# Optimization experiments

Hardware: AMD Instinct MI355X
Metric: run time of the kernel (lower is better)

## Reference

```python
import jax, jax.numpy as jnp
import numpy as np

B, C, CI, H, W = 8, 1024, 512, 56, 56
BN_EPS = 1e-5


def _conv1x1(x, w, b):
    # x: [B,C,H,W], w: [O,C], b: [O] -> [B,O,H,W]
    return jnp.einsum('bchw,oc->bohw', x, w) + b[None, :, None, None]


def setup_inputs() -> dict:
    key = jax.random.key(0)
    ks = jax.random.split(key, 12)
    s = lambda k, shape: (jax.random.normal(k, shape, jnp.float32) * 0.02)
    return {
        'x': jax.random.normal(ks[0], (B, C, H, W), jnp.float32),
        'theta_w': s(ks[1], (CI, C)), 'theta_b': s(ks[2], (CI,)),
        'phi_w': s(ks[3], (CI, C)), 'phi_b': s(ks[4], (CI,)),
        'g_w': s(ks[5], (CI, C)), 'g_b': s(ks[6], (CI,)),
        'wz_w': s(ks[7], (C, CI)), 'wz_b': s(ks[8], (C,)),
        'bn_gamma': 1.0 + 0.1 * jax.random.normal(ks[9], (C,), jnp.float32),
        'bn_beta': s(ks[10], (C,)),
    }


def reference(x, theta_w, theta_b, phi_w, phi_b, g_w, g_b, wz_w, wz_b, bn_gamma, bn_beta):
    b, c, h, w = x.shape
    n = h * w
    # 1x1-conv projections, flattened to token sequences
    g_x = _conv1x1(x, g_w, g_b).reshape(b, -1, n).transpose(0, 2, 1)       # [B,N,CI]
    theta_x = _conv1x1(x, theta_w, theta_b).reshape(b, -1, n).transpose(0, 2, 1)  # [B,N,CI]
    phi_x = _conv1x1(x, phi_w, phi_b).reshape(b, -1, n)                     # [B,CI,N]
    # embedded-gaussian: f = theta @ phi^T, softmax over last dim
    f = jnp.einsum('bnc,bcm->bnm', theta_x, phi_x)                          # [B,N,N]
    attn = jax.nn.softmax(f, axis=-1)
    y = jnp.einsum('bnm,bmc->bnc', attn, g_x)                               # [B,N,CI]
    y = y.transpose(0, 2, 1).reshape(b, -1, h, w)                           # [B,CI,H,W]
    z = _conv1x1(y, wz_w, wz_b)                                             # [B,C,H,W]
    # BatchNorm2d in training mode: batch statistics over (B,H,W), biased var
    mean = z.mean(axis=(0, 2, 3))
    var = z.var(axis=(0, 2, 3))
    zn = (z - mean[None, :, None, None]) * jax.lax.rsqrt(var + BN_EPS)[None, :, None, None]
    zn = zn * bn_gamma[None, :, None, None] + bn_beta[None, :, None, None]
    return zn + x
```

## Files before the change

kernel.cpp:

```cpp
#include <hip/hip_runtime.h>
#include <cstdint>
#include <cstdio>

#define DEVINL __device__ __forceinline__

typedef _Float16 f16x8 __attribute__((ext_vector_type(8)));
typedef float    f32x4 __attribute__((ext_vector_type(4)));

static constexpr int B_  = 8;
static constexpr int C_  = 1024;
static constexpr int CI_ = 512;
static constexpr int N_  = 56 * 56;
static constexpr int NP  = 3328;
static constexpr float BN_EPS = 1e-5f;

DEVINL uint16_t f2h(float f) {
  union { _Float16 h; uint16_t u; } cv;
  cv.h = (_Float16)f;
  return cv.u;
}

DEVINL void async16(const void* g, void* lds) {
  __builtin_amdgcn_global_load_lds(
      (const __attribute__((address_space(1))) uint32_t*)g,
      (__attribute__((address_space(3))) uint32_t*)lds, 16, 0, 0);
}

template <int BIAS>
__global__ __launch_bounds__(512, 2) void gemm256(
    const uint16_t* __restrict__ A, const uint16_t* __restrict__ Bt,
    uint16_t* __restrict__ Cc, const float* __restrict__ bias,
    int K, int lda, int ldb, int ldc,
    long aBatch, long bBatch, long cBatch, int nbx, int nby, int colMajor) {
  __shared__ uint16_t lds[65536];

  const int nwg = gridDim.x, orig = blockIdx.x;
  const int q = nwg >> 3, r = nwg & 7, xcd = orig & 7, idx = orig >> 3;
  const int wgid = (xcd < r ? xcd * (q + 1) : r * (q + 1) + (xcd - r) * q) + idx;
  const int rest = wgid % (nbx * nby);
  const int bx = colMajor ? rest / nby : rest % nbx;
  const int by = colMajor ? rest % nby : rest / nbx;
  const int zb = wgid / (nbx * nby);

  const int tid = threadIdx.x, w = tid >> 6, l = tid & 63;
  const int wm = w >> 2, wn = w & 3, lr = l & 15, lg = l >> 4;

  const uint16_t* Ab = A + (long)zb * aBatch + (long)bx * 256 * lda;
  const uint16_t* Bb = Bt + (long)zb * bBatch + (long)by * 256 * ldb;

  const int NT = K >> 6;

  const int c0 = tid, c1 = 512 + tid;
  const long aoff0 = (long)(c0 >> 2) * lda + (((c0 & 3) ^ ((c0 >> 3) & 3)) * 8);
  const long aoff1 = (long)(c1 >> 2) * lda + (((c1 & 3) ^ ((c1 >> 3) & 3)) * 8);
  const long boff0 = (long)(c0 >> 2) * ldb + (((c0 & 3) ^ ((c0 >> 3) & 3)) * 8);
  const long boff1 = (long)(c1 >> 2) * ldb + (((c1 & 3) ^ ((c1 >> 3) & 3)) * 8);
  const int ldsW0 = (w * 64) * 8;
  const int ldsW1 = (512 + w * 64) * 8;

  auto stageA = [&](int t, int ks, int buf) {
    int tw = t; while (tw >= NT) tw -= NT;
    const uint16_t* src = Ab + tw * 64 + ks * 32;
    const int reg = (buf * 2 + ks) * 8192;
    async16(src + aoff0, &lds[reg + ldsW0]);
    async16(src + aoff1, &lds[reg + ldsW1]);
  };
  auto stageB = [&](int t, int ks, int buf) {
    int tw = t; while (tw >= NT) tw -= NT;
    const uint16_t* src = Bb + tw * 64 + ks * 32;
    const int reg = 32768 + (buf * 2 + ks) * 8192;
    async16(src + boff0, &lds[reg + ldsW0]);
    async16(src + boff1, &lds[reg + ldsW1]);
  };

  const int laneSwz = (lg ^ ((lr >> 1) & 3)) * 8;
  f32x4 acc[8][4] = {};
  f16x8 af[4], bf[4];

#define LOAD_A(b, ks, mh)                                                     \
  _Pragma("unroll") for (int i = 0; i < 4; ++i) {                             \
    const int row_ = wm * 128 + ((mh) * 4 + i) * 16 + lr;                     \
    af[i] = *reinterpret_cast<const f16x8*>(                                  \
        &lds[((b) * 2 + (ks)) * 8192 + row_ * 32 + laneSwz]);                 \
  }
#define LOAD_B(b, ks)                                                         \
  _Pragma("unroll") for (int i = 0; i < 4; ++i) {                             \
    const int row_ = wn * 64 + i * 16 + lr;                                   \
    bf[i] = *reinterpret_cast<const f16x8*>(                                  \
        &lds[32768 + ((b) * 2 + (ks)) * 8192 + row_ * 32 + laneSwz]);         \
  }
#define MFMA16(mh)                                                            \
  _Pragma("unroll") for (int i = 0; i < 4; ++i)                               \
  _Pragma("unroll") for (int j = 0; j < 4; ++j)                               \
    acc[(mh) * 4 + i][j] = __builtin_amdgcn_mfma_f32_16x16x32_f16(            \
        af[i], bf[j], acc[(mh) * 4 + i][j], 0, 0, 0);
#define WAIT_LGKM()                                       \
  asm volatile("s_waitcnt lgkmcnt(0)" ::: "memory");      \
  __builtin_amdgcn_sched_barrier(0);
#define WAIT_VM8()                                        \
  asm volatile("s_waitcnt vmcnt(8)" ::: "memory");        \
  __builtin_amdgcn_sched_barrier(0);

#define TILE(t, b)                                                            \
  {                                                                           \
                                                   \
    LOAD_B(b, 0); LOAD_A(b, 0, 0);                                            \
    stageA((t) + 1, 1, (b) ^ 1);                                              \
    __builtin_amdgcn_s_barrier(); WAIT_LGKM();                                \
    __builtin_amdgcn_s_setprio(1); MFMA16(0); __builtin_amdgcn_s_setprio(0);  \
    __builtin_amdgcn_s_barrier();                                             \
                                                   \
    LOAD_A(b, 0, 1);                                                          \
    stageB((t) + 1, 1, (b) ^ 1);                                              \
    __builtin_amdgcn_s_barrier(); WAIT_LGKM();                                \
    __builtin_amdgcn_s_setprio(1); MFMA16(1); __builtin_amdgcn_s_setprio(0);  \
    WAIT_VM8();                                                               \
    __builtin_amdgcn_s_barrier();                                             \
                                                   \
    LOAD_B(b, 1); LOAD_A(b, 1, 0);                                            \
    stageA((t) + 2, 0, (b));                                                  \
    __builtin_amdgcn_s_barrier(); WAIT_LGKM();                                \
    __builtin_amdgcn_s_setprio(1); MFMA16(0); __builtin_amdgcn_s_setprio(0);  \
    __builtin_amdgcn_s_barrier();                                             \
                                                   \
    LOAD_A(b, 1, 1);                                                          \
    stageB((t) + 2, 0, (b));                                                  \
    __builtin_amdgcn_s_barrier(); WAIT_LGKM();                                \
    __builtin_amdgcn_s_setprio(1); MFMA16(1); __builtin_amdgcn_s_setprio(0);  \
    WAIT_VM8();                                                               \
    __builtin_amdgcn_s_barrier();                                             \
  }

  stageA(0, 0, 0); stageB(0, 0, 0);
  stageA(0, 1, 0); stageB(0, 1, 0);
  stageA(1, 0, 1); stageB(1, 0, 1);
  WAIT_VM8();
  __builtin_amdgcn_s_barrier();

  const int NTE = NT & ~1;
  for (int tp = 0; tp < NTE; tp += 2) {
    TILE(tp, 0);
    TILE(tp + 1, 1);
  }
  if (NT & 1) TILE(NT - 1, 0);

#undef TILE
#undef LOAD_A
#undef LOAD_B
#undef MFMA16
#undef WAIT_LGKM
#undef WAIT_VM8

  uint16_t* Cp = Cc + (long)zb * cBatch + ((long)bx * 256) * ldc + (long)by * 256;
#pragma unroll
  for (int mf = 0; mf < 8; ++mf) {
#pragma unroll
    for (int nf = 0; nf < 4; ++nf) {
      const int col = wn * 64 + nf * 16 + lr;
      const f32x4 v = acc[mf][nf];
#pragma unroll
      for (int qq = 0; qq < 4; ++qq) {
        const int row = wm * 128 + mf * 16 + lg * 4 + qq;
        float val = v[qq];
        if constexpr (BIAS == 1) val += bias[bx * 256 + row];
        if constexpr (BIAS == 2) val += bias[by * 256 + col];
        Cp[(long)row * ldc + col] = f2h(val);
      }
    }
  }
}

__global__ __launch_bounds__(256) void transpose_cast(
    const float* __restrict__ x, uint16_t* __restrict__ xT) {
  __shared__ float t[32][33];
  const int b = blockIdx.z;
  const float* xb = x + (long)b * C_ * N_;
  uint16_t* xTb = xT + (long)b * NP * C_;
  const int n0 = blockIdx.x * 32, c0 = blockIdx.y * 32;
  const int tx = threadIdx.x & 31, ty = threadIdx.x >> 5;
#pragma unroll
  for (int i = 0; i < 4; ++i) {
    const int cc = c0 + ty + i * 8, nn = n0 + tx;
    t[ty + i * 8][tx] = (nn < N_) ? xb[(long)cc * N_ + nn] : 0.f;
  }
  __syncthreads();
#pragma unroll
  for (int i = 0; i < 4; ++i) {
    const int nn = n0 + ty + i * 8, cc = c0 + tx;
    xTb[(long)nn * C_ + cc] = f2h(t[tx][ty + i * 8]);
  }
}

__global__ __launch_bounds__(256) void cvt_f16_all(
    const float* __restrict__ s0, uint16_t* __restrict__ d0, int n0,
    const float* __restrict__ s1, uint16_t* __restrict__ d1, int n1,
    const float* __restrict__ s2, uint16_t* __restrict__ d2, int n2,
    const float* __restrict__ s3, uint16_t* __restrict__ d3, int n3) {
  const int stride = gridDim.x * 256;
  const int total = n0 + n1 + n2 + n3;
  for (int i = blockIdx.x * 256 + threadIdx.x; i < total; i += stride) {
    int j = i;
    if (j < n0) { d0[j] = f2h(s0[j]); continue; }
    j -= n0;
    if (j < n1) { d1[j] = f2h(s1[j]); continue; }
    j -= n1;
    if (j < n2) { d2[j] = f2h(s2[j]); continue; }
    j -= n2;
    d3[j] = f2h(s3[j]);
  }
}

__global__ __launch_bounds__(256) void concat_bias(
    const float* __restrict__ a, const float* __restrict__ b,
    float* __restrict__ d) {
  const int i = blockIdx.x * 256 + threadIdx.x;
  if (i < 512) d[i] = a[i];
  else if (i < 1024) d[i] = b[i - 512];
}

__global__ __launch_bounds__(256) void softmax_inplace(uint16_t* __restrict__ f) {
  const int row = blockIdx.x, tid = threadIdx.x;
  uint16_t* p = f + ((long)blockIdx.y * NP + row) * NP;
  __shared__ float buf[N_];
  __shared__ float red[8];
  float mx = -3.4e38f;
  for (int ch = tid; ch < N_ / 8; ch += 256) {
    const f16x8 v = *reinterpret_cast<const f16x8*>(p + ch * 8);
#pragma unroll
    for (int j = 0; j < 8; ++j) {
      const float fv = (float)v[j];
      buf[ch * 8 + j] = fv;
      mx = fmaxf(mx, fv);
    }
  }
  for (int o = 32; o; o >>= 1) mx = fmaxf(mx, __shfl_xor(mx, o));
  if ((tid & 63) == 0) red[tid >> 6] = mx;
  __syncthreads();
  mx = fmaxf(fmaxf(red[0], red[1]), fmaxf(red[2], red[3]));

  float s = 0.f;
  for (int i = tid; i < N_; i += 256) {
    const float e = __expf(buf[i] - mx);
    buf[i] = e;
    s += e;
  }
  for (int o = 32; o; o >>= 1) s += __shfl_xor(s, o);
  __syncthreads();
  if ((tid & 63) == 0) red[tid >> 6] = s;
  __syncthreads();
  const float rinv = 1.0f / (red[0] + red[1] + red[2] + red[3]);

  for (int ch = tid; ch < N_ / 8; ch += 256) {
    f16x8 o8;
#pragma unroll
    for (int j = 0; j < 8; ++j) o8[j] = (_Float16)(buf[ch * 8 + j] * rinv);
    *reinterpret_cast<f16x8*>(p + ch * 8) = o8;
  }
}

__global__ __launch_bounds__(256) void bn_stats(
    const _Float16* __restrict__ z, const float* __restrict__ gamma,
    const float* __restrict__ beta, float* __restrict__ ss) {
  const int c = blockIdx.x, tid = threadIdx.x;
  float sum = 0.f, sq = 0.f;
  for (int b = 0; b < B_; ++b) {
    const _Float16* zp = z + ((long)b * C_ + c) * NP;
    for (int ch = tid; ch < N_ / 8; ch += 256) {
      const f16x8 v = *(const f16x8*)(zp + ch * 8);
#pragma unroll
      for (int j = 0; j < 8; ++j) {
        const float fv = (float)v[j];
        sum += fv;
        sq += fv * fv;
      }
    }
  }
  for (int o = 32; o; o >>= 1) {
    sum += __shfl_xor(sum, o);
    sq += __shfl_xor(sq, o);
  }
  __shared__ float r1[8], r2[8];
  if ((tid & 63) == 0) { r1[tid >> 6] = sum; r2[tid >> 6] = sq; }
  __syncthreads();
  if (tid == 0) {
    sum = r1[0] + r1[1] + r1[2] + r1[3];
    sq  = r2[0] + r2[1] + r2[2] + r2[3];
    const float inv_n = 1.0f / (float)(B_ * N_);
    const float mean = sum * inv_n;
    const float var = sq * inv_n - mean * mean;
    const float sc = gamma[c] * rsqrtf(var + BN_EPS);
    ss[c] = sc;
    ss[C_ + c] = beta[c] - mean * sc;
  }
}

__global__ __launch_bounds__(256) void bn_apply(
    const _Float16* __restrict__ z, const float* __restrict__ x,
    const float* __restrict__ ss, float* __restrict__ out) {
  constexpr int CH = N_ / 8;
  const long nv = (long)B_ * C_ * CH;
  const long stride = (long)gridDim.x * 256;
  for (long v = (long)blockIdx.x * 256 + threadIdx.x; v < nv; v += stride) {
    const long row = v / CH;
    const int ch = (int)(v % CH);
    const int c = (int)(row % C_);
    const f16x8 zz = *(const f16x8*)(z + row * NP + ch * 8);
    const f32x4 x0 = *(const f32x4*)(x + row * (long)N_ + ch * 8);
    const f32x4 x1 = *(const f32x4*)(x + row * (long)N_ + ch * 8 + 4);
    const float sc = ss[c], sh = ss[C_ + c];
    f32x4 o0, o1;
#pragma unroll
    for (int j = 0; j < 4; ++j) o0[j] = (float)zz[j] * sc + sh + x0[j];
#pragma unroll
    for (int j = 0; j < 4; ++j) o1[j] = (float)zz[4 + j] * sc + sh + x1[j];
    __builtin_nontemporal_store(o0, (f32x4*)(out + row * (long)N_ + ch * 8));
    __builtin_nontemporal_store(o1, (f32x4*)(out + row * (long)N_ + ch * 8 + 4));
  }
}

extern "C" void kernel_launch(void* const* d_in, const int* in_sizes, int n_in,
                              void* d_out, int out_size, void* d_ws,
                              size_t ws_size, hipStream_t stream) {
  const float* x       = (const float*)d_in[0];
  const float* theta_w = (const float*)d_in[1];
  const float* theta_b = (const float*)d_in[2];
  const float* phi_w   = (const float*)d_in[3];
  const float* phi_b   = (const float*)d_in[4];
  const float* g_w     = (const float*)d_in[5];
  const float* g_b     = (const float*)d_in[6];
  const float* wz_w    = (const float*)d_in[7];
  const float* wz_b    = (const float*)d_in[8];
  const float* gamma   = (const float*)d_in[9];
  const float* beta    = (const float*)d_in[10];
  float* out = (float*)d_out;

  char* ws = (char*)d_ws;
  size_t off = 0;
  auto alloc = [&](size_t bytes) {
    void* p = ws + off;
    off += (bytes + 255) & ~(size_t)255;
    return p;
  };
  uint16_t* wfused = (uint16_t*)alloc((size_t)1024 * 1024 * 2);
  uint16_t* wg     = (uint16_t*)alloc((size_t)CI_ * C_ * 2);
  uint16_t* wzh    = (uint16_t*)alloc((size_t)C_ * CI_ * 2);
  float*    bfused = (float*)alloc((size_t)1024 * 4);
  uint16_t* projT  = (uint16_t*)alloc((size_t)B_ * NP * 1024 * 2);
  uint16_t* gbuf   = (uint16_t*)alloc((size_t)B_ * CI_ * NP * 2);
  uint16_t* ybuf   = (uint16_t*)alloc((size_t)B_ * NP * CI_ * 2);
  uint16_t* zbuf   = (uint16_t*)alloc((size_t)B_ * C_ * NP * 2);
  float*    ss     = (float*)alloc((size_t)C_ * 2 * 4);

  const size_t xTb = (size_t)B_ * NP * C_ * 2;
  const size_t fB  = (size_t)B_ * NP * NP * 2;
  uint16_t* xT    = (uint16_t*)alloc(fB > xTb ? fB : xTb);
  uint16_t* fattn = xT;
  if (off > ws_size) {
    fprintf(stderr, "kernel_launch: workspace too small: need %zu have %zu\n",
            off, ws_size);
    return;
  }

  cvt_f16_all<<<512, 256, 0, stream>>>(
      theta_w, wfused, CI_ * C_,
      phi_w, wfused + 512 * 1024, CI_ * C_,
      g_w, wg, CI_ * C_,
      wz_w, wzh, C_ * CI_);
  concat_bias<<<4, 256, 0, stream>>>(theta_b, phi_b, bfused);

  transpose_cast<<<dim3(NP / 32, C_ / 32, B_), 256, 0, stream>>>(x, xT);

  gemm256<2><<<dim3(B_ * NP / 256 * 4), 512, 0, stream>>>(
      xT, wfused, projT, bfused, C_, C_, C_, 1024,
      0, 0, 0, B_ * NP / 256, 4, 1);
  gemm256<1><<<dim3(2 * 13 * B_), 512, 0, stream>>>(
      wg, xT, gbuf, g_b, C_, C_, C_, NP,
      0, (long)NP * C_, (long)CI_ * NP, 2, 13, 0);

  gemm256<0><<<dim3(13 * 13 * B_), 512, 0, stream>>>(
      projT, projT + 512, fattn, nullptr, CI_, 1024, 1024, NP,
      (long)NP * 1024, (long)NP * 1024, (long)NP * NP, 13, 13, 0);
  softmax_inplace<<<dim3(N_, B_), 256, 0, stream>>>(fattn);

  gemm256<0><<<dim3(13 * 2 * B_), 512, 0, stream>>>(
      fattn, gbuf, ybuf, nullptr, N_, NP, NP, CI_,
      (long)NP * NP, (long)CI_ * NP, (long)NP * CI_, 13, 2, 1);

  gemm256<1><<<dim3(4 * 13 * B_), 512, 0, stream>>>(
      wzh, ybuf, zbuf, wz_b, CI_, CI_, CI_, NP,
      0, (long)NP * CI_, (long)C_ * NP, 4, 13, 0);

  bn_stats<<<C_, 256, 0, stream>>>((const _Float16*)zbuf, gamma, beta, ss);
  bn_apply<<<4096, 256, 0, stream>>>((const _Float16*)zbuf, x, ss, out);
}
```

Before: 508.1 us.

## Fuse softmax exponentiation into attention-value GEMM A-tile staging

The softmax pass no longer writes normalized probabilities back to the score matrix. It only computes the row max and the reciprocal sum. The attn@g GEMM now exponentiates the raw score tiles in LDS after they are staged, and scales its output rows by the reciprocal sum in the epilogue. This avoids one full read-modify-write of the B×N×N fp16 score matrix. The cost is an extra LDS pass with exp work and an added barrier per K sub-tile inside the GEMM main loop, and the padded score columns must now be safe to exponentiate.

```diff
diff --git a/kernel.cpp b/kernel.cpp
--- a/kernel.cpp
+++ b/kernel.cpp
@@ -26,12 +26,14 @@
       (__attribute__((address_space(3))) uint32_t*)lds, 16, 0, 0);
 }
 
-template <int BIAS>
+template <int BIAS, int EXPA>
 __global__ __launch_bounds__(512, 2) void gemm256(
     const uint16_t* __restrict__ A, const uint16_t* __restrict__ Bt,
     uint16_t* __restrict__ Cc, const float* __restrict__ bias,
     int K, int lda, int ldb, int ldc,
-    long aBatch, long bBatch, long cBatch, int nbx, int nby, int colMajor) {
+    long aBatch, long bBatch, long cBatch, int nbx, int nby, int colMajor,
+    const float* __restrict__ rowM, const float* __restrict__ rowScale,
+    long rmBatch) {
   __shared__ uint16_t lds[65536];
 
   const int nwg = gridDim.x, orig = blockIdx.x;
@@ -49,6 +51,15 @@
   const uint16_t* Bb = Bt + (long)zb * bBatch + (long)by * 256 * ldb;
 
   const int NT = K >> 6;
+
+  float mA0 = 0.f, mA1 = 0.f;
+  const float* rscB = nullptr;
+  if constexpr (EXPA) {
+    const float* rm = rowM + (long)zb * rmBatch + (long)bx * 256;
+    mA0 = rm[tid >> 2];
+    mA1 = rm[128 + (tid >> 2)];
+    rscB = rowScale + (long)zb * rmBatch + (long)bx * 256;
+  }
 
   const int c0 = tid, c1 = 512 + tid;
   const long aoff0 = (long)(c0 >> 2) * lda + (((c0 & 3) ^ ((c0 >> 3) & 3)) * 8);
@@ -100,9 +111,26 @@
 #define WAIT_VM8()                                        \
   asm volatile("s_waitcnt vmcnt(8)" ::: "memory");        \
   __builtin_amdgcn_sched_barrier(0);
+#define PREP(b, ks)                                                           \
+  if constexpr (EXPA) {                                                       \
+    const int base_ = ((b) * 2 + (ks)) * 8192;                                \
+    f16x8 v0_ = *reinterpret_cast<const f16x8*>(&lds[base_ + tid * 8]);       \
+    f16x8 v1_ = *reinterpret_cast<const f16x8*>(&lds[base_ + (512 + tid) * 8]);\
+    f16x8 o0_, o1_;                                                           \
+    _Pragma("unroll") for (int j = 0; j < 8; ++j) {                           \
+      o0_[j] = (_Float16)__expf((float)v0_[j] - mA0);                         \
+      o1_[j] = (_Float16)__expf((float)v1_[j] - mA1);                         \
+    }                                                                         \
+    *reinterpret_cast<f16x8*>(&lds[base_ + tid * 8]) = o0_;                   \
+    *reinterpret_cast<f16x8*>(&lds[base_ + (512 + tid) * 8]) = o1_;           \
+    asm volatile("s_waitcnt lgkmcnt(0)" ::: "memory");                        \
+    __builtin_amdgcn_sched_barrier(0);                                        \
+    __builtin_amdgcn_s_barrier();                                             \
+  }
 
 #define TILE(t, b)                                                            \
   {                                                                           \
+    PREP(b, 0)                                                                \
                                                    \
     LOAD_B(b, 0); LOAD_A(b, 0, 0);                                            \
     stageA((t) + 1, 1, (b) ^ 1);                                              \
@@ -116,6 +144,7 @@
     __builtin_amdgcn_s_setprio(1); MFMA16(1); __builtin_amdgcn_s_setprio(0);  \
     WAIT_VM8();                                                               \
     __builtin_amdgcn_s_barrier();                                             \
+    PREP(b, 1)                                                                \
                                                    \
     LOAD_B(b, 1); LOAD_A(b, 1, 0);                                            \
     stageA((t) + 2, 0, (b));                                                  \
@@ -145,6 +174,7 @@
   if (NT & 1) TILE(NT - 1, 0);
 
 #undef TILE
+#undef PREP
 #undef LOAD_A
 #undef LOAD_B
 #undef MFMA16
@@ -164,6 +194,7 @@
         float val = v[qq];
         if constexpr (BIAS == 1) val += bias[bx * 256 + row];
         if constexpr (BIAS == 2) val += bias[by * 256 + col];
+        if constexpr (EXPA) val *= rscB[row];
         Cp[(long)row * ldc + col] = f2h(val);
       }
     }
@@ -218,9 +249,16 @@
   else if (i < 1024) d[i] = b[i - 512];
 }
 
-__global__ __launch_bounds__(256) void softmax_inplace(uint16_t* __restrict__ f) {
+__global__ __launch_bounds__(256) void rowstat(
+    const uint16_t* __restrict__ f, float* __restrict__ rowM,
+    float* __restrict__ rowScale) {
   const int row = blockIdx.x, tid = threadIdx.x;
-  uint16_t* p = f + ((long)blockIdx.y * NP + row) * NP;
+  const long g = (long)blockIdx.y * NP + row;
+  if (row >= N_) {
+    if (tid == 0) { rowM[g] = 3.4e38f; rowScale[g] = 0.f; }
+    return;
+  }
+  const uint16_t* p = f + g * NP;
   __shared__ float buf[N_];
   __shared__ float red[8];
   float mx = -3.4e38f;
@@ -239,22 +277,14 @@
   mx = fmaxf(fmaxf(red[0], red[1]), fmaxf(red[2], red[3]));
 
   float s = 0.f;
-  for (int i = tid; i < N_; i += 256) {
-    const float e = __expf(buf[i] - mx);
-    buf[i] = e;
-    s += e;
-  }
+  for (int i = tid; i < N_; i += 256) s += __expf(buf[i] - mx);
   for (int o = 32; o; o >>= 1) s += __shfl_xor(s, o);
   __syncthreads();
   if ((tid & 63) == 0) red[tid >> 6] = s;
   __syncthreads();
-  const float rinv = 1.0f / (red[0] + red[1] + red[2] + red[3]);
-
-  for (int ch = tid; ch < N_ / 8; ch += 256) {
-    f16x8 o8;
-#pragma unroll
-    for (int j = 0; j < 8; ++j) o8[j] = (_Float16)(buf[ch * 8 + j] * rinv);
-    *reinterpret_cast<f16x8*>(p + ch * 8) = o8;
+  if (tid == 0) {
+    rowM[g] = mx;
+    rowScale[g] = 1.0f / (red[0] + red[1] + red[2] + red[3]);
   }
 }
 
@@ -350,6 +380,8 @@
   uint16_t* ybuf   = (uint16_t*)alloc((size_t)B_ * NP * CI_ * 2);
   uint16_t* zbuf   = (uint16_t*)alloc((size_t)B_ * C_ * NP * 2);
   float*    ss     = (float*)alloc((size_t)C_ * 2 * 4);
+  float*    rowM   = (float*)alloc((size_t)B_ * NP * 4);
+  float*    rowSc  = (float*)alloc((size_t)B_ * NP * 4);
 
   const size_t xTb = (size_t)B_ * NP * C_ * 2;
   const size_t fB  = (size_t)B_ * NP * NP * 2;
@@ -370,25 +402,27 @@
 
   transpose_cast<<<dim3(NP / 32, C_ / 32, B_), 256, 0, stream>>>(x, xT);
 
-  gemm256<2><<<dim3(B_ * NP / 256 * 4), 512, 0, stream>>>(
+  gemm256<2, 0><<<dim3(B_ * NP / 256 * 4), 512, 0, stream>>>(
       xT, wfused, projT, bfused, C_, C_, C_, 1024,
-      0, 0, 0, B_ * NP / 256, 4, 1);
-  gemm256<1><<<dim3(2 * 13 * B_), 512, 0, stream>>>(
+      0, 0, 0, B_ * NP / 256, 4, 1, nullptr, nullptr, 0);
+  gemm256<1, 0><<<dim3(2 * 13 * B_), 512, 0, stream>>>(
       wg, xT, gbuf, g_b, C_, C_, C_, NP,
-      0, (long)NP * C_, (long)CI_ * NP, 2, 13, 0);
-
-  gemm256<0><<<dim3(13 * 13 * B_), 512, 0, stream>>>(
+      0, (long)NP * C_, (long)CI_ * NP, 2, 13, 0, nullptr, nullptr, 0);
+
+  gemm256<0, 0><<<dim3(13 * 13 * B_), 512, 0, stream>>>(
       projT, projT + 512, fattn, nullptr, CI_, 1024, 1024, NP,
-      (long)NP * 1024, (long)NP * 1024, (long)NP * NP, 13, 13, 0);
-  softmax_inplace<<<dim3(N_, B_), 256, 0, stream>>>(fattn);
-
-  gemm256<0><<<dim3(13 * 2 * B_), 512, 0, stream>>>(
+      (long)NP * 1024, (long)NP * 1024, (long)NP * NP, 13, 13, 0,
+      nullptr, nullptr, 0);
+  rowstat<<<dim3(NP, B_), 256, 0, stream>>>(fattn, rowM, rowSc);
+
+  gemm256<0, 1><<<dim3(13 * 2 * B_), 512, 0, stream>>>(
       fattn, gbuf, ybuf, nullptr, N_, NP, NP, CI_,
-      (long)NP * NP, (long)CI_ * NP, (long)NP * CI_, 13, 2, 1);
-
-  gemm256<1><<<dim3(4 * 13 * B_), 512, 0, stream>>>(
+      (long)NP * NP, (long)CI_ * NP, (long)NP * CI_, 13, 2, 1,
+      rowM, rowSc, NP);
+
+  gemm256<1, 0><<<dim3(4 * 13 * B_), 512, 0, stream>>>(
       wzh, ybuf, zbuf, wz_b, CI_, CI_, CI_, NP,
-      0, (long)NP * CI_, (long)C_ * NP, 4, 13, 0);
+      0, (long)NP * CI_, (long)C_ * NP, 4, 13, 0, nullptr, nullptr, 0);
 
   bn_stats<<<C_, 256, 0, stream>>>((const _Float16*)zbuf, gamma, beta, ss);
   bn_apply<<<4096, 256, 0, stream>>>((const _Float16*)zbuf, x, ss, out);
```

Measured after the change: 523.1 us. 1.03x slower.
